# Performance work log

Measured on AMD Instinct MI355X. Metric: run time of the kernel, lower is better.

Reference implementation:

```python
import jax, jax.numpy as jnp
import numpy as np

B, S, D, U, L, DEG = 32, 256, 256, 256, 16, 16
N = B * S
E = N * DEG


def _xavier(k, shape, fan_in, fan_out):
    return jax.random.normal(k, shape, jnp.float32) * np.float32(np.sqrt(2.0 / (fan_in + fan_out)))


def setup_inputs() -> dict:
    key = jax.random.key(0)
    ks = jax.random.split(key, 16)
    src = jax.random.normal(ks[0], (S, B, D), jnp.float32)
    V_in = _xavier(ks[1], (L, D, U), D, U)
    b_in = jnp.zeros((L, U), jnp.float32)
    V_in_gate = _xavier(ks[2], (D, 1), D, 1)
    b_in_gate = jnp.ones((L, 1), jnp.float32)
    V_out = _xavier(ks[3], (L, D, U), D, U)
    b_out = jnp.zeros((L, U), jnp.float32)
    V_out_gate = _xavier(ks[4], (D, 1), D, 1)
    b_out_gate = jnp.ones((L, 1), jnp.float32)
    W_self_loop = _xavier(ks[5], (D, U), D, U)
    W_self_loop_gate = _xavier(ks[6], (D, 1), D, 1)
    arc_tensor_in = jnp.stack([jax.random.randint(ks[7], (E,), 0, B),
                               jax.random.randint(ks[8], (E,), 0, S)]).astype(jnp.int64)
    arc_tensor_out = jnp.stack([jax.random.randint(ks[9], (E,), 0, B),
                                jax.random.randint(ks[10], (E,), 0, S)]).astype(jnp.int64)
    label_tensor_in = jax.random.randint(ks[11], (1, E), 0, L).astype(jnp.int64)
    label_tensor_out = jax.random.randint(ks[12], (1, E), 0, L).astype(jnp.int64)
    mask_in = jnp.ones((N, DEG), jnp.float32)
    mask_out = jnp.ones((N, DEG), jnp.float32)
    mask_loop = jnp.ones((N, 1), jnp.float32)
    sent_mask = jnp.ones((S, B), jnp.float32)
    return {"src": src, "V_in": V_in, "b_in": b_in, "V_in_gate": V_in_gate,
            "b_in_gate": b_in_gate, "V_out": V_out, "b_out": b_out,
            "V_out_gate": V_out_gate, "b_out_gate": b_out_gate,
            "W_self_loop": W_self_loop, "W_self_loop_gate": W_self_loop_gate,
            "arc_tensor_in": arc_tensor_in, "arc_tensor_out": arc_tensor_out,
            "label_tensor_in": label_tensor_in, "label_tensor_out": label_tensor_out,
            "mask_in": mask_in, "mask_out": mask_out, "mask_loop": mask_loop,
            "sent_mask": sent_mask}


def _gcn_forward(src, V_in, b_in, V_in_gate, b_in_gate, V_out, b_out, V_out_gate,
                 b_out_gate, W_self_loop, W_self_loop_gate, mask_in, mask_out,
                 mask_loop, sent_mask, arc_tensor_in, arc_tensor_out,
                 label_tensor_in, label_tensor_out):
    S_, B_, D_ = src.shape
    U_ = V_in.shape[-1]
    enc = jnp.transpose(src, (1, 0, 2))            # [B,S,D]
    x = enc.reshape(B_ * S_, D_)                   # [N,D]

    def arc_branch(V, b, Vg, bg, arc, lab):
        # per-label transform of all nodes, as in the original: [L,N,U]
        all_lab = jnp.einsum('nd,ldu->lnu', x, V)
        idx = arc[0] * S_ + arc[1]                 # [E] flat node indices
        l = lab[0]                                  # [E] edge labels
        feats = all_lab[l, idx] + b[l]              # [E,U]
        deg = idx.shape[0] // (B_ * S_)
        feats = feats.reshape(B_, S_, deg, U_)
        g = (x @ Vg)[idx, 0] + bg[l, 0]             # [E]
        gate = g.reshape(B_, S_, deg)
        return feats, gate

    in_, in_gate = arc_branch(V_in, b_in, V_in_gate, b_in_gate, arc_tensor_in, label_tensor_in)
    out_, out_gate = arc_branch(V_out, b_out, V_out_gate, b_out_gate, arc_tensor_out, label_tensor_out)
    same = (x @ W_self_loop).reshape(B_, S_, 1, U_)
    same_gate = (x @ W_self_loop_gate).reshape(B_, S_, 1)

    pot = jnp.concatenate([in_, out_, same], axis=2)            # [B,S,maxdeg,U]
    pot_gate = jnp.concatenate([in_gate, out_gate, same_gate], axis=2)
    mask_soft = jnp.concatenate([mask_in, mask_out, mask_loop], axis=1)  # [N,maxdeg]
    md = pot.shape[2]
    pot = pot.reshape(B_ * S_, md, U_)
    probs = jax.nn.sigmoid(pot_gate.reshape(B_ * S_, md)) * mask_soft
    res = jax.nn.relu(jnp.sum(pot * probs[:, :, None], axis=1)).reshape(B_, S_, U_)
    res = res * sent_mask.T[:, :, None]
    return jnp.transpose(res, (1, 0, 2))            # [S,B,U]


def reference(src, V_in, b_in, V_in_gate, b_in_gate, V_out, b_out, V_out_gate,
              b_out_gate, W_self_loop, W_self_loop_gate, arc_tensor_in,
              arc_tensor_out, label_tensor_in, label_tensor_out, mask_in,
              mask_out, mask_loop, sent_mask):
    return _gcn_forward(src, V_in, b_in, V_in_gate, b_in_gate, V_out, b_out,
                        V_out_gate, b_out_gate, W_self_loop, W_self_loop_gate,
                        mask_in, mask_out, mask_loop, sent_mask,
                        arc_tensor_in, arc_tensor_out, label_tensor_in,
                        label_tensor_out)
```

## Files before the change

kernel.cpp:

```cpp
#include <hip/hip_runtime.h>
#include <hip/hip_bf16.h>

#define BB 32
#define SS 256
#define DD 256
#define UU 256
#define LL 16
#define DEG 16
#define NN (BB * SS)
#define EE (NN * DEG)
#define NSLICE 33
#define KMAIN (NSLICE * DD)
#define KEXT 256
#define KTOT (KMAIN + KEXT)
#define KSPLIT 8
#define KS (KTOT / KSPLIT)

using short8 = __attribute__((ext_vector_type(8))) short;
using f32x4  = __attribute__((ext_vector_type(4))) float;

#define GLDS(g, l)                                                        \
  __builtin_amdgcn_global_load_lds(                                       \
      (const __attribute__((address_space(1))) void*)(g),                 \
      (__attribute__((address_space(3))) void*)(l), 16, 0, 0)

__device__ __forceinline__ float bf2f(unsigned short v) {
  union { unsigned u; float f; } t;
  t.u = ((unsigned)v) << 16;
  return t.f;
}
__device__ __forceinline__ unsigned short f2bf(float f) {
  __hip_bfloat16 h = __float2bfloat16(f);
  return *(unsigned short*)&h;
}
__device__ __forceinline__ float sigm(float x) {
  return 1.f / (1.f + __expf(-x));
}

__global__ __launch_bounds__(256) void k_prep(
    const float* __restrict__ src, const float* __restrict__ gin,
    const float* __restrict__ gout, const float* __restrict__ gloop,
    __hip_bfloat16* __restrict__ x_bf, float* __restrict__ xg_in,
    float* __restrict__ xg_out, float* __restrict__ xg_loop) {
  int n = blockIdx.x;
  int b = n / SS, s = n % SS;
  int d = threadIdx.x;
  float v = src[(size_t)(s * BB + b) * DD + d];
  x_bf[(size_t)n * DD + d] = __float2bfloat16(v);
  float p0 = v * gin[d], p1 = v * gout[d], p2 = v * gloop[d];
#pragma unroll
  for (int o = 32; o > 0; o >>= 1) {
    p0 += __shfl_down(p0, o);
    p1 += __shfl_down(p1, o);
    p2 += __shfl_down(p2, o);
  }
  __shared__ float r0[4], r1[4], r2[4];
  int w = threadIdx.x >> 6, lane = threadIdx.x & 63;
  if (lane == 0) { r0[w] = p0; r1[w] = p1; r2[w] = p2; }
  __syncthreads();
  if (threadIdx.x == 0) {
    xg_in[n]   = r0[0] + r0[1] + r0[2] + r0[3];
    xg_out[n]  = r1[0] + r1[1] + r1[2] + r1[3];
    xg_loop[n] = r2[0] + r2[1] + r2[2] + r2[3];
  }
}

__global__ void k_transpose(const float* __restrict__ Vin,
                            const float* __restrict__ Vout,
                            const float* __restrict__ Wself,
                            const float* __restrict__ b_in,
                            const float* __restrict__ b_out,
                            __hip_bfloat16* __restrict__ Vt) {
  int z = blockIdx.z;
  int tx = threadIdx.x, ty = threadIdx.y;
  if (z == NSLICE) {
    int u0 = blockIdx.x * 32, j0 = blockIdx.y * 32;
#pragma unroll
    for (int i = 0; i < 4; i++) {
      int u = u0 + ty + i * 8, j = j0 + tx;
      float v = 0.f;
      if (j >= 1 && j <= LL)         v = b_in[(j - 1) * UU + u];
      else if (j > LL && j < NSLICE) v = b_out[(j - 1 - LL) * UU + u];
      Vt[(size_t)u * KTOT + KMAIN + j] = __float2bfloat16(v);
    }
    return;
  }
  __shared__ float t[32][33];
  const float* srcM = (z == 0) ? Wself
                    : (z <= LL ? Vin  + (size_t)(z - 1)      * DD * UU
                               : Vout + (size_t)(z - 1 - LL) * DD * UU);
  int u0 = blockIdx.x * 32, d0 = blockIdx.y * 32;
#pragma unroll
  for (int i = 0; i < 4; i++) {
    int dr = ty + i * 8;
    t[dr][tx] = srcM[(size_t)(d0 + dr) * UU + u0 + tx];
  }
  __syncthreads();
#pragma unroll
  for (int i = 0; i < 4; i++) {
    int ur = ty + i * 8;
    Vt[(size_t)(u0 + ur) * KTOT + z * DD + d0 + tx] = __float2bfloat16(t[tx][ur]);
  }
}

__global__ __launch_bounds__(64) void k_agg(
    const __hip_bfloat16* __restrict__ x,
    const float* __restrict__ xg_in, const float* __restrict__ xg_out,
    const float* __restrict__ xg_loop,
    const float* __restrict__ b_ing, const float* __restrict__ b_outg,
    const int* __restrict__ arc_in, const int* __restrict__ arc_out,
    const int* __restrict__ lab_in, const int* __restrict__ lab_out,
    const float* __restrict__ mask_in, const float* __restrict__ mask_out,
    const float* __restrict__ mask_loop,
    __hip_bfloat16* __restrict__ Y) {
  __shared__ int u_sl[32], u_src[32];
  __shared__ float u_w[32];
  __shared__ int s_sl[32], s_src[32];
  __shared__ float s_w[32];
  __shared__ float s_wsum[NSLICE];
  int n = blockIdx.x, tid = threadIdx.x;
  if (tid < 32) {
    int br = tid >> 4, k = tid & 15;
    int e = n * DEG + k;
    const int* a = br ? arc_out : arc_in;
    int l = (br ? lab_out : lab_in)[e];
    int srcn = a[e] * SS + a[EE + e];
    float g = (br ? xg_out : xg_in)[srcn] + (br ? b_outg : b_ing)[l];
    u_sl[tid] = 1 + br * LL + l;
    u_src[tid] = srcn;
    u_w[tid] = sigm(g) * (br ? mask_out : mask_in)[e];
  }
  __syncthreads();
  if (tid < 32) {
    int my = u_sl[tid];
    int rank = 0;
#pragma unroll
    for (int j = 0; j < 32; j++) {
      int oj = u_sl[j];
      rank += (oj < my || (oj == my && j < tid)) ? 1 : 0;
    }
    s_sl[rank] = my;
    s_src[rank] = u_src[tid];
    s_w[rank] = u_w[tid];
  }
  __syncthreads();

  const unsigned short* xp = (const unsigned short*)x;
  unsigned short* yp = (unsigned short*)Y;
  size_t base = (size_t)n * KTOT;
  int d4 = tid * 4;
  {
    float wl = sigm(xg_loop[n]) * mask_loop[n];
    ushort4 v = *(const ushort4*)&xp[(size_t)n * DD + d4];
    ushort4 o;
    o.x = f2bf(wl * bf2f(v.x)); o.y = f2bf(wl * bf2f(v.y));
    o.z = f2bf(wl * bf2f(v.z)); o.w = f2bf(wl * bf2f(v.w));
    *(ushort4*)&yp[base + d4] = o;
  }
  unsigned long long present = 0ull;
  float a0 = 0.f, a1 = 0.f, a2 = 0.f, a3 = 0.f, ws = 0.f;
#pragma unroll
  for (int e = 0; e < 32; e++) {
    int sl = s_sl[e];
    int srcn = s_src[e];
    float w = s_w[e];
    ushort4 v = *(const ushort4*)&xp[(size_t)srcn * DD + d4];
    a0 += w * bf2f(v.x); a1 += w * bf2f(v.y);
    a2 += w * bf2f(v.z); a3 += w * bf2f(v.w);
    ws += w;
    int slnext = (e < 31) ? s_sl[e + 1] : 999;
    if (sl != slnext) {
      ushort4 o;
      o.x = f2bf(a0); o.y = f2bf(a1); o.z = f2bf(a2); o.w = f2bf(a3);
      *(ushort4*)&yp[base + sl * DD + d4] = o;
      if (tid == 0) s_wsum[sl] = ws;
      present |= (1ull << sl);
      a0 = a1 = a2 = a3 = ws = 0.f;
    }
  }
  ushort4 zero4 = {0, 0, 0, 0};
#pragma unroll
  for (int s = 1; s < NSLICE; s++) {
    if (!((present >> s) & 1ull)) {
      *(ushort4*)&yp[base + s * DD + d4] = zero4;
      if (tid == 0) s_wsum[s] = 0.f;
    }
  }
  __syncthreads();
  {
    ushort4 o;
    unsigned short* op = (unsigned short*)&o;
#pragma unroll
    for (int c = 0; c < 4; c++) {
      int j = d4 + c;
      float v = (j >= 1 && j < NSLICE) ? s_wsum[j] : 0.f;
      op[c] = f2bf(v);
    }
    *(ushort4*)&yp[base + KMAIN + d4] = o;
  }
}

__global__ __launch_bounds__(256) void k_gemm(
    const __hip_bfloat16* __restrict__ A, const __hip_bfloat16* __restrict__ Bt,
    __hip_bfloat16* __restrict__ partial) {
  __shared__ __align__(16) __hip_bfloat16 As[128 * 32];
  __shared__ __align__(16) __hip_bfloat16 Bs[128 * 32];
  __hip_bfloat16* P = partial + (size_t)blockIdx.z * NN * UU;
  int kbeg = blockIdx.z * KS;

  int row0 = blockIdx.x * 128, col0 = blockIdx.y * 128;
  int tid = threadIdx.x;
  int w = tid >> 6, lane = tid & 63;
  int wr = (w >> 1) * 64, wc = (w & 1) * 64;
  int lrow = lane & 15, quad = lane >> 4;
  int sr = lane >> 2;
  int sc = (lane & 3) * 8;

  f32x4 acc[4][4] = {};
  for (int k0 = kbeg; k0 < kbeg + KS; k0 += 32) {
#pragma unroll
    for (int t = 0; t < 2; t++) {
      int rb = (w * 2 + t) * 16;
      GLDS(&A[(size_t)(row0 + rb + sr) * KTOT + k0 + sc], &As[rb * 32]);
      GLDS(&Bt[(size_t)(col0 + rb + sr) * KTOT + k0 + sc], &Bs[rb * 32]);
    }
    __syncthreads();
    short8 af[4], bfr[4];
#pragma unroll
    for (int i = 0; i < 4; i++)
      af[i] = *(const short8*)&As[(wr + i * 16 + lrow) * 32 + quad * 8];
#pragma unroll
    for (int j = 0; j < 4; j++)
      bfr[j] = *(const short8*)&Bs[(wc + j * 16 + lrow) * 32 + quad * 8];
#pragma unroll
    for (int i = 0; i < 4; i++)
#pragma unroll
      for (int j = 0; j < 4; j++)
        acc[i][j] = __builtin_amdgcn_mfma_f32_16x16x32_bf16(af[i], bfr[j], acc[i][j], 0, 0, 0);
    __syncthreads();
  }
#pragma unroll
  for (int i = 0; i < 4; i++)
#pragma unroll
    for (int j = 0; j < 4; j++) {
      int col = col0 + wc + j * 16 + lrow;
      int rowb = row0 + wr + i * 16 + quad * 4;
#pragma unroll
      for (int r = 0; r < 4; r++)
        P[(size_t)(rowb + r) * UU + col] = __float2bfloat16(acc[i][j][r]);
    }
}

__global__ __launch_bounds__(64) void k_finish(
    const __hip_bfloat16* __restrict__ partial, const float* __restrict__ sent,
    float* __restrict__ out) {
  int n = blockIdx.x, u4 = threadIdx.x * 4;
  size_t idx = (size_t)n * UU + u4;
  const unsigned short* pp = (const unsigned short*)partial;
  float a0 = 0.f, a1 = 0.f, a2 = 0.f, a3 = 0.f;
#pragma unroll
  for (int z = 0; z < KSPLIT; z++) {
    ushort4 v = *(const ushort4*)&pp[(size_t)z * NN * UU + idx];
    a0 += bf2f(v.x); a1 += bf2f(v.y); a2 += bf2f(v.z); a3 += bf2f(v.w);
  }
  int s = n % SS, b = n / SS;
  float sm = sent[s * BB + b];
  float4 o;
  o.x = fmaxf(a0, 0.f) * sm; o.y = fmaxf(a1, 0.f) * sm;
  o.z = fmaxf(a2, 0.f) * sm; o.w = fmaxf(a3, 0.f) * sm;
  *(float4*)&out[((size_t)s * BB + b) * UU + u4] = o;
}

extern "C" void kernel_launch(void* const* d_in, const int* in_sizes, int n_in,
                              void* d_out, int out_size, void* d_ws, size_t ws_size,
                              hipStream_t stream) {
  const float* src      = (const float*)d_in[0];
  const float* V_in     = (const float*)d_in[1];
  const float* b_in     = (const float*)d_in[2];
  const float* V_ing    = (const float*)d_in[3];
  const float* b_ing    = (const float*)d_in[4];
  const float* V_out    = (const float*)d_in[5];
  const float* b_out    = (const float*)d_in[6];
  const float* V_outg   = (const float*)d_in[7];
  const float* b_outg   = (const float*)d_in[8];
  const float* W_self   = (const float*)d_in[9];
  const float* W_selfg  = (const float*)d_in[10];
  const int* arc_in     = (const int*)d_in[11];
  const int* arc_out    = (const int*)d_in[12];
  const int* lab_in     = (const int*)d_in[13];
  const int* lab_out    = (const int*)d_in[14];
  const float* mask_in  = (const float*)d_in[15];
  const float* mask_out = (const float*)d_in[16];
  const float* mask_loop= (const float*)d_in[17];
  const float* sent     = (const float*)d_in[18];
  float* out = (float*)d_out;

  char* ws = (char*)d_ws;
  size_t off = 0;
  auto alloc = [&](size_t bytes) -> void* {
    void* p = ws + off;
    off += (bytes + 255) & ~(size_t)255;
    return p;
  };
  __hip_bfloat16* x_bf = (__hip_bfloat16*)alloc((size_t)NN * DD * 2);
  __hip_bfloat16* Vt   = (__hip_bfloat16*)alloc((size_t)UU * KTOT * 2);
  float* xg_in   = (float*)alloc(NN * 4);
  float* xg_out  = (float*)alloc(NN * 4);
  float* xg_loop = (float*)alloc(NN * 4);
  __hip_bfloat16* Y = (__hip_bfloat16*)alloc((size_t)NN * KTOT * 2);
  __hip_bfloat16* partial =
      (__hip_bfloat16*)alloc((size_t)KSPLIT * NN * UU * 2);

  k_prep<<<NN, 256, 0, stream>>>(src, V_ing, V_outg, W_selfg, x_bf, xg_in, xg_out, xg_loop);
  k_transpose<<<dim3(UU / 32, DD / 32, NSLICE + 1), dim3(32, 8), 0, stream>>>(
      V_in, V_out, W_self, b_in, b_out, Vt);
  k_agg<<<NN, 64, 0, stream>>>(x_bf, xg_in, xg_out, xg_loop, b_ing, b_outg,
                               arc_in, arc_out, lab_in, lab_out,
                               mask_in, mask_out, mask_loop, Y);
  k_gemm<<<dim3(NN / 128, UU / 128, KSPLIT), 256, 0, stream>>>(Y, Vt, partial);
  k_finish<<<NN, 64, 0, stream>>>(partial, sent, out);
}
```

Before: 210.9 us.

## Double-buffer GEMM with full-width N tile and merge prep/transpose kernels

The GEMM now covers the full U=256 width per block (128x256 tile), so each A tile is loaded once instead of twice. It double-buffers LDS so the next K-slice's global-to-LDS loads overlap the current MFMAs, with one barrier per iteration instead of two. The prep and weight-transpose kernels are merged into one launch to remove a kernel boundary. The cost is higher register pressure (32 accumulators per thread) and more LDS per block, which may limit occupancy.

```diff
diff --git a/kernel.cpp b/kernel.cpp
--- a/kernel.cpp
+++ b/kernel.cpp
@@ -15,6 +15,8 @@
 #define KTOT (KMAIN + KEXT)
 #define KSPLIT 8
 #define KS (KTOT / KSPLIT)
+#define TM 128
+#define TN 256
 
 using short8 = __attribute__((ext_vector_type(8))) short;
 using f32x4  = __attribute__((ext_vector_type(4))) float;
@@ -37,44 +39,48 @@
   return 1.f / (1.f + __expf(-x));
 }
 
-__global__ __launch_bounds__(256) void k_prep(
+__global__ __launch_bounds__(256) void k_pre(
     const float* __restrict__ src, const float* __restrict__ gin,
     const float* __restrict__ gout, const float* __restrict__ gloop,
+    const float* __restrict__ Vin, const float* __restrict__ Vout,
+    const float* __restrict__ Wself, const float* __restrict__ b_in,
+    const float* __restrict__ b_out,
     __hip_bfloat16* __restrict__ x_bf, float* __restrict__ xg_in,
-    float* __restrict__ xg_out, float* __restrict__ xg_loop) {
-  int n = blockIdx.x;
-  int b = n / SS, s = n % SS;
-  int d = threadIdx.x;
-  float v = src[(size_t)(s * BB + b) * DD + d];
-  x_bf[(size_t)n * DD + d] = __float2bfloat16(v);
-  float p0 = v * gin[d], p1 = v * gout[d], p2 = v * gloop[d];
-#pragma unroll
-  for (int o = 32; o > 0; o >>= 1) {
-    p0 += __shfl_down(p0, o);
-    p1 += __shfl_down(p1, o);
-    p2 += __shfl_down(p2, o);
-  }
-  __shared__ float r0[4], r1[4], r2[4];
-  int w = threadIdx.x >> 6, lane = threadIdx.x & 63;
-  if (lane == 0) { r0[w] = p0; r1[w] = p1; r2[w] = p2; }
-  __syncthreads();
-  if (threadIdx.x == 0) {
-    xg_in[n]   = r0[0] + r0[1] + r0[2] + r0[3];
-    xg_out[n]  = r1[0] + r1[1] + r1[2] + r1[3];
-    xg_loop[n] = r2[0] + r2[1] + r2[2] + r2[3];
-  }
-}
-
-__global__ void k_transpose(const float* __restrict__ Vin,
-                            const float* __restrict__ Vout,
-                            const float* __restrict__ Wself,
-                            const float* __restrict__ b_in,
-                            const float* __restrict__ b_out,
-                            __hip_bfloat16* __restrict__ Vt) {
-  int z = blockIdx.z;
-  int tx = threadIdx.x, ty = threadIdx.y;
+    float* __restrict__ xg_out, float* __restrict__ xg_loop,
+    __hip_bfloat16* __restrict__ Vt) {
+  int bid = blockIdx.x;
+  if (bid < NN) {
+    int n = bid;
+    int b = n / SS, s = n % SS;
+    int d = threadIdx.x;
+    float v = src[(size_t)(s * BB + b) * DD + d];
+    x_bf[(size_t)n * DD + d] = __float2bfloat16(v);
+    float p0 = v * gin[d], p1 = v * gout[d], p2 = v * gloop[d];
+#pragma unroll
+    for (int o = 32; o > 0; o >>= 1) {
+      p0 += __shfl_down(p0, o);
+      p1 += __shfl_down(p1, o);
+      p2 += __shfl_down(p2, o);
+    }
+    __shared__ float r0[4], r1[4], r2[4];
+    int w = threadIdx.x >> 6, lane = threadIdx.x & 63;
+    if (lane == 0) { r0[w] = p0; r1[w] = p1; r2[w] = p2; }
+    __syncthreads();
+    if (threadIdx.x == 0) {
+      xg_in[n]   = r0[0] + r0[1] + r0[2] + r0[3];
+      xg_out[n]  = r1[0] + r1[1] + r1[2] + r1[3];
+      xg_loop[n] = r2[0] + r2[1] + r2[2] + r2[3];
+    }
+    return;
+  }
+  int t = bid - NN;
+  int z = t >> 6;
+  int rem = t & 63;
+  int bx = rem & 7, by = rem >> 3;
+  int tid = threadIdx.x;
+  int tx = tid & 31, ty = tid >> 5;
   if (z == NSLICE) {
-    int u0 = blockIdx.x * 32, j0 = blockIdx.y * 32;
+    int u0 = bx * 32, j0 = by * 32;
 #pragma unroll
     for (int i = 0; i < 4; i++) {
       int u = u0 + ty + i * 8, j = j0 + tx;
@@ -85,21 +91,21 @@
     }
     return;
   }
-  __shared__ float t[32][33];
+  __shared__ float tbuf[32][33];
   const float* srcM = (z == 0) ? Wself
                     : (z <= LL ? Vin  + (size_t)(z - 1)      * DD * UU
                                : Vout + (size_t)(z - 1 - LL) * DD * UU);
-  int u0 = blockIdx.x * 32, d0 = blockIdx.y * 32;
+  int u0 = bx * 32, d0 = by * 32;
 #pragma unroll
   for (int i = 0; i < 4; i++) {
     int dr = ty + i * 8;
-    t[dr][tx] = srcM[(size_t)(d0 + dr) * UU + u0 + tx];
+    tbuf[dr][tx] = srcM[(size_t)(d0 + dr) * UU + u0 + tx];
   }
   __syncthreads();
 #pragma unroll
   for (int i = 0; i < 4; i++) {
     int ur = ty + i * 8;
-    Vt[(size_t)(u0 + ur) * KTOT + z * DD + d0 + tx] = __float2bfloat16(t[tx][ur]);
+    Vt[(size_t)(u0 + ur) * KTOT + z * DD + d0 + tx] = __float2bfloat16(tbuf[tx][ur]);
   }
 }
 
@@ -200,51 +206,62 @@
   }
 }
 
-__global__ __launch_bounds__(256) void k_gemm(
+__global__ __launch_bounds__(256, 2) void k_gemm(
     const __hip_bfloat16* __restrict__ A, const __hip_bfloat16* __restrict__ Bt,
     __hip_bfloat16* __restrict__ partial) {
-  __shared__ __align__(16) __hip_bfloat16 As[128 * 32];
-  __shared__ __align__(16) __hip_bfloat16 Bs[128 * 32];
-  __hip_bfloat16* P = partial + (size_t)blockIdx.z * NN * UU;
-  int kbeg = blockIdx.z * KS;
-
-  int row0 = blockIdx.x * 128, col0 = blockIdx.y * 128;
+  __shared__ __align__(16) __hip_bfloat16 As[2][TM * 32];
+  __shared__ __align__(16) __hip_bfloat16 Bs[2][TN * 32];
+  __hip_bfloat16* P = partial + (size_t)blockIdx.y * NN * UU;
+  int kbeg = blockIdx.y * KS;
+  int row0 = blockIdx.x * TM;
   int tid = threadIdx.x;
   int w = tid >> 6, lane = tid & 63;
-  int wr = (w >> 1) * 64, wc = (w & 1) * 64;
   int lrow = lane & 15, quad = lane >> 4;
   int sr = lane >> 2;
   int sc = (lane & 3) * 8;
 
-  f32x4 acc[4][4] = {};
-  for (int k0 = kbeg; k0 < kbeg + KS; k0 += 32) {
-#pragma unroll
-    for (int t = 0; t < 2; t++) {
-      int rb = (w * 2 + t) * 16;
-      GLDS(&A[(size_t)(row0 + rb + sr) * KTOT + k0 + sc], &As[rb * 32]);
-      GLDS(&Bt[(size_t)(col0 + rb + sr) * KTOT + k0 + sc], &Bs[rb * 32]);
-    }
+#define STAGE(bufi, k0)                                                     \
+  {                                                                         \
+    _Pragma("unroll")                                                       \
+    for (int t = 0; t < 2; t++) {                                           \
+      int rb = (w * 2 + t) * 16;                                            \
+      GLDS(&A[(size_t)(row0 + rb + sr) * KTOT + (k0) + sc],                 \
+           &As[bufi][rb * 32]);                                             \
+    }                                                                       \
+    _Pragma("unroll")                                                       \
+    for (int t = 0; t < 4; t++) {                                           \
+      int rb = (w * 4 + t) * 16;                                            \
+      GLDS(&Bt[(size_t)(rb + sr) * KTOT + (k0) + sc], &Bs[bufi][rb * 32]);  \
+    }                                                                       \
+  }
+
+  STAGE(0, kbeg);
+  f32x4 acc[8][4] = {};
+  constexpr int NIT = KS / 32;
+  for (int it = 0; it < NIT; it++) {
+    int cur = it & 1;
     __syncthreads();
-    short8 af[4], bfr[4];
-#pragma unroll
-    for (int i = 0; i < 4; i++)
-      af[i] = *(const short8*)&As[(wr + i * 16 + lrow) * 32 + quad * 8];
+    if (it + 1 < NIT) STAGE(cur ^ 1, kbeg + (it + 1) * 32);
+    short8 af[8], bfr[4];
+#pragma unroll
+    for (int i = 0; i < 8; i++)
+      af[i] = *(const short8*)&As[cur][(i * 16 + lrow) * 32 + quad * 8];
 #pragma unroll
     for (int j = 0; j < 4; j++)
-      bfr[j] = *(const short8*)&Bs[(wc + j * 16 + lrow) * 32 + quad * 8];
-#pragma unroll
-    for (int i = 0; i < 4; i++)
-#pragma unroll
-      for (int j = 0; j < 4; j++)
+      bfr[j] = *(const short8*)&Bs[cur][(w * 64 + j * 16 + lrow) * 32 + quad * 8];
+#pragma unroll
+    for (int j = 0; j < 4; j++)
+#pragma unroll
+      for (int i = 0; i < 8; i++)
         acc[i][j] = __builtin_amdgcn_mfma_f32_16x16x32_bf16(af[i], bfr[j], acc[i][j], 0, 0, 0);
-    __syncthreads();
-  }
-#pragma unroll
-  for (int i = 0; i < 4; i++)
+  }
+#undef STAGE
+#pragma unroll
+  for (int i = 0; i < 8; i++)
 #pragma unroll
     for (int j = 0; j < 4; j++) {
-      int col = col0 + wc + j * 16 + lrow;
-      int rowb = row0 + wr + i * 16 + quad * 4;
+      int col = w * 64 + j * 16 + lrow;
+      int rowb = row0 + i * 16 + quad * 4;
 #pragma unroll
       for (int r = 0; r < 4; r++)
         P[(size_t)(rowb + r) * UU + col] = __float2bfloat16(acc[i][j][r]);
@@ -311,12 +328,12 @@
   __hip_bfloat16* partial =
       (__hip_bfloat16*)alloc((size_t)KSPLIT * NN * UU * 2);
 
-  k_prep<<<NN, 256, 0, stream>>>(src, V_ing, V_outg, W_selfg, x_bf, xg_in, xg_out, xg_loop);
-  k_transpose<<<dim3(UU / 32, DD / 32, NSLICE + 1), dim3(32, 8), 0, stream>>>(
-      V_in, V_out, W_self, b_in, b_out, Vt);
+  k_pre<<<NN + (NSLICE + 1) * 64, 256, 0, stream>>>(
+      src, V_ing, V_outg, W_selfg, V_in, V_out, W_self, b_in, b_out,
+      x_bf, xg_in, xg_out, xg_loop, Vt);
   k_agg<<<NN, 64, 0, stream>>>(x_bf, xg_in, xg_out, xg_loop, b_ing, b_outg,
                                arc_in, arc_out, lab_in, lab_out,
                                mask_in, mask_out, mask_loop, Y);
-  k_gemm<<<dim3(NN / 128, UU / 128, KSPLIT), 256, 0, stream>>>(Y, Vt, partial);
+  k_gemm<<<dim3(NN / TM, KSPLIT), 256, 0, stream>>>(Y, Vt, partial);
   k_finish<<<NN, 64, 0, stream>>>(partial, sent, out);
 }
```

Result: faster. 192.4 us (-8.8%).
